# Performance work log

Hardware: AMD Instinct MI355X
Metric: run time of the kernel (lower is better)

## Reference

```python
import jax, jax.numpy as jnp
import numpy as np

D_MODEL = 1024
VOCAB = 32000
NUM_HEADS = 3  # MTP steps
NHEAD = 2      # attention heads per encoder layer
D_FF = 2048    # torch TransformerEncoderLayer default dim_feedforward
EPS_RMS = 1e-8
EPS_LN = 1e-5


def rmsnorm(x):
    rms = jnp.sqrt(jnp.mean(x * x, axis=-1, keepdims=True) + EPS_RMS)
    return x / rms


def layernorm(x, g, b):
    m = jnp.mean(x, axis=-1, keepdims=True)
    v = jnp.mean((x - m) ** 2, axis=-1, keepdims=True)
    return (x - m) / jnp.sqrt(v + EPS_LN) * g + b


def encoder_layer_single_token(x, p):
    # x: (..., d). Self-attention over a length-1 sequence: softmax over one key
    # gives attention weight 1, so attn_out = Wo @ (Wv @ x). Post-norm (torch default).
    v = x @ p['Wv'].T + p['bv']
    attn = v @ p['Wo'].T + p['bo']
    x = layernorm(x + attn, p['ln1_g'], p['ln1_b'])
    ff = jax.nn.relu(x @ p['W1'].T + p['b1']) @ p['W2'].T + p['b2']
    x = layernorm(x + ff, p['ln2_g'], p['ln2_b'])
    return x


def setup_inputs() -> dict:
    key = jax.random.key(0)
    ks = jax.random.split(key, 4)
    token_ids = jax.random.randint(ks[0], (4, 512), 0, VOCAB)
    embed = jax.random.normal(ks[1], (VOCAB, D_MODEL), dtype=jnp.float32) * 0.02
    s = 1.0 / np.sqrt(D_MODEL)
    params = []
    kk = ks[2]
    for k in range(NUM_HEADS):
        kk, *sub = jax.random.split(kk, 10)
        p = {
            'Wmerge': jax.random.normal(sub[0], (D_MODEL, 2 * D_MODEL)) * s,
            'bmerge': jnp.zeros((D_MODEL,)),
            'Wv': jax.random.normal(sub[1], (D_MODEL, D_MODEL)) * s,
            'bv': jnp.zeros((D_MODEL,)),
            'Wo': jax.random.normal(sub[2], (D_MODEL, D_MODEL)) * s,
            'bo': jnp.zeros((D_MODEL,)),
            'W1': jax.random.normal(sub[3], (D_FF, D_MODEL)) * s,
            'b1': jnp.zeros((D_FF,)),
            'W2': jax.random.normal(sub[4], (D_MODEL, D_FF)) * (1.0 / np.sqrt(D_FF)),
            'b2': jnp.zeros((D_MODEL,)),
            'ln1_g': jnp.ones((D_MODEL,)), 'ln1_b': jnp.zeros((D_MODEL,)),
            'ln2_g': jnp.ones((D_MODEL,)), 'ln2_b': jnp.zeros((D_MODEL,)),
        }
        params.append(p)
    # flatten params into dict entries layer{k}_{name}
    out = {'token_ids': token_ids, 'embed': embed}
    for k, p in enumerate(params):
        for name, val in p.items():
            out[f'l{k}_{name}'] = val
    return out


def _forward(token_ids, embed, layers):
    B, T = token_ids.shape
    embeds = embed[token_ids]              # (B, T, d)
    n_pos = T - NUM_HEADS                  # positions i = 0 .. T-NUM_HEADS-1
    # vectorize over i: h_prev starts as h0_seq[:, i, :] for all i at once
    idx = jnp.arange(n_pos)
    h_prev = embeds[:, idx, :]             # (B, P, d)
    logits_list = []
    for k in range(NUM_HEADS):
        p = layers[k]
        tok = embeds[:, idx + (k + 1), :]  # (B, P, d) future token embeds
        merged = jnp.concatenate([rmsnorm(h_prev), rmsnorm(tok)], axis=-1)  # (B,P,2d)
        x = merged @ p['Wmerge'].T + p['bmerge']                            # (B,P,d)
        h_curr = encoder_layer_single_token(x, p)
        logits = h_curr @ embed.T          # tied unembed (B,P,V)
        logits_list.append(logits)
        h_prev = h_curr
    # stack -> (B, P, NUM_HEADS, V) matching torch stack(dim=1) per-position then outer list
    return jnp.stack(logits_list, axis=2)


def reference(token_ids, embed,
              l0_Wmerge, l0_bmerge, l0_Wv, l0_bv, l0_Wo, l0_bo, l0_W1, l0_b1, l0_W2, l0_b2, l0_ln1_g, l0_ln1_b, l0_ln2_g, l0_ln2_b,
              l1_Wmerge, l1_bmerge, l1_Wv, l1_bv, l1_Wo, l1_bo, l1_W1, l1_b1, l1_W2, l1_b2, l1_ln1_g, l1_ln1_b, l1_ln2_g, l1_ln2_b,
              l2_Wmerge, l2_bmerge, l2_Wv, l2_bv, l2_Wo, l2_bo, l2_W1, l2_b1, l2_W2, l2_b2, l2_ln1_g, l2_ln1_b, l2_ln2_g, l2_ln2_b):
    names = ['Wmerge', 'bmerge', 'Wv', 'bv', 'Wo', 'bo', 'W1', 'b1', 'W2', 'b2', 'ln1_g', 'ln1_b', 'ln2_g', 'ln2_b']
    vals = [l0_Wmerge, l0_bmerge, l0_Wv, l0_bv, l0_Wo, l0_bo, l0_W1, l0_b1, l0_W2, l0_b2, l0_ln1_g, l0_ln1_b, l0_ln2_g, l0_ln2_b,
            l1_Wmerge, l1_bmerge, l1_Wv, l1_bv, l1_Wo, l1_bo, l1_W1, l1_b1, l1_W2, l1_b2, l1_ln1_g, l1_ln1_b, l1_ln2_g, l1_ln2_b,
            l2_Wmerge, l2_bmerge, l2_Wv, l2_bv, l2_Wo, l2_bo, l2_W1, l2_b1, l2_W2, l2_b2, l2_ln1_g, l2_ln1_b, l2_ln2_g, l2_ln2_b]
    layers = [dict(zip(names, vals[i * 14:(i + 1) * 14])) for i in range(NUM_HEADS)]
    return _forward(token_ids, embed, layers)
```

## Files before the change

### kernel.cpp

```cpp
#include <hip/hip_runtime.h>


#define NPOS   509
#define MROWS  2036
#define MPAD   2048
#define DMODEL 1024

typedef _Float16 f16;
typedef _Float16 f16x8 __attribute__((ext_vector_type(8)));
typedef _Float16 f16x4 __attribute__((ext_vector_type(4)));
typedef float    f32x4 __attribute__((ext_vector_type(4)));

#define MFMA16(a, b, c) __builtin_amdgcn_mfma_f32_16x16x32_f16(a, b, c, 0, 0, 0)
#define VM0  asm volatile("s_waitcnt vmcnt(0)" ::: "memory")
#define VM2  asm volatile("s_waitcnt vmcnt(2)" ::: "memory")
#define VM10 asm volatile("s_waitcnt vmcnt(10)" ::: "memory")
#define BAR  asm volatile("s_barrier" ::: "memory")

__device__ __forceinline__ void gld_lds16(const void* g, void* l) {
  __builtin_amdgcn_global_load_lds(
      (const __attribute__((address_space(1))) void*)g,
      (__attribute__((address_space(3))) void*)l, 16, 0, 0);
}

__global__ __launch_bounds__(256) void conv_f32_f16(const float* __restrict__ src,
                                                    f16* __restrict__ dst, long n) {
  long i = ((long)blockIdx.x * 256 + threadIdx.x) * 8;
  if (i + 8 <= n) {
    float4 a = *(const float4*)(src + i);
    float4 b = *(const float4*)(src + i + 4);
    f16x8 o = {(f16)a.x, (f16)a.y, (f16)a.z, (f16)a.w,
               (f16)b.x, (f16)b.y, (f16)b.z, (f16)b.w};
    *(f16x8*)(dst + i) = o;
  }
}

struct ConvArgs { const float* s[12]; f16* d[12]; long n[12]; };
__global__ __launch_bounds__(256) void conv_many(ConvArgs a) {
  int t = blockIdx.y;
  long i = ((long)blockIdx.x * 256 + threadIdx.x) * 8;
  if (i + 8 <= a.n[t]) {
    const float* src = a.s[t];
    float4 x = *(const float4*)(src + i);
    float4 y = *(const float4*)(src + i + 4);
    f16x8 o = {(f16)x.x, (f16)x.y, (f16)x.z, (f16)x.w,
               (f16)y.x, (f16)y.y, (f16)y.z, (f16)y.w};
    *(f16x8*)(a.d[t] + i) = o;
  }
}

struct TpArgs { const float* s[3]; f16* d[3]; };
__global__ __launch_bounds__(256) void transpose3(TpArgs a) {
  __shared__ float t[32][33];
  int h = blockIdx.z;
  int bx = blockIdx.x * 32, by = blockIdx.y * 32;
  int tx = threadIdx.x & 31, ty = threadIdx.x >> 5;
  const float* src = a.s[h];
  f16* dst = a.d[h];
  #pragma unroll
  for (int r = 0; r < 32; r += 8)
    t[ty + r][tx] = src[(long)(by + ty + r) * 1024 + bx + tx];
  __syncthreads();
  #pragma unroll
  for (int r = 0; r < 32; r += 8)
    dst[(long)(bx + ty + r) * 1024 + by + tx] = (f16)t[tx][ty + r];
}

struct BvoArgs { const float* Wo[3]; const float* bv[3]; const float* bo[3]; float* out[3]; };
__global__ __launch_bounds__(64) void make_bvo3(BvoArgs a) {
  int h = blockIdx.y, r = blockIdx.x, l = threadIdx.x;
  const float* Wo = a.Wo[h];
  const float* bv = a.bv[h];
  float s = 0.0f;
  for (int k = l; k < 1024; k += 64) s += Wo[(long)r * 1024 + k] * bv[k];
  #pragma unroll
  for (int off = 32; off > 0; off >>= 1) s += __shfl_xor(s, off);
  if (l == 0) a.out[h][r] = s + a.bo[h][r];
}

__device__ __forceinline__ float2 block_reduce2(float a, float b) {
  #pragma unroll
  for (int off = 32; off > 0; off >>= 1) {
    a += __shfl_xor(a, off);
    b += __shfl_xor(b, off);
  }
  __shared__ float2 red[4];
  int wv = threadIdx.x >> 6;
  if ((threadIdx.x & 63) == 0) red[wv] = make_float2(a, b);
  __syncthreads();
  float2 r0 = red[0], r1 = red[1], r2 = red[2], r3 = red[3];
  return make_float2(r0.x + r1.x + r2.x + r3.x, r0.y + r1.y + r2.y + r3.y);
}

__global__ __launch_bounds__(256) void merge_rms(const float* __restrict__ hprev,
                                                 const float* __restrict__ embed,
                                                 const int* __restrict__ tok,
                                                 f16* __restrict__ merged, int koff,
                                                 int hsel) {
  int r = blockIdx.x;
  int b = r / NPOS, t = r - b * NPOS;
  int tid = threadIdx.x;
  const float* hrow = (hsel >= 0)
      ? embed + (long)tok[b * 512 + t + hsel] * DMODEL
      : hprev + (long)r * DMODEL;
  float4 hv = ((const float4*)hrow)[tid];
  float4 tv = ((const float4*)(embed + (long)tok[b * 512 + t + koff] * DMODEL))[tid];
  float sh = hv.x * hv.x + hv.y * hv.y + hv.z * hv.z + hv.w * hv.w;
  float st = tv.x * tv.x + tv.y * tv.y + tv.z * tv.z + tv.w * tv.w;
  float2 tot = block_reduce2(sh, st);
  float ih = 1.0f / sqrtf(tot.x * (1.0f / DMODEL) + 1e-8f);
  float it = 1.0f / sqrtf(tot.y * (1.0f / DMODEL) + 1e-8f);
  f16x4 oh = {(f16)(hv.x * ih), (f16)(hv.y * ih), (f16)(hv.z * ih), (f16)(hv.w * ih)};
  f16x4 ot = {(f16)(tv.x * it), (f16)(tv.y * it), (f16)(tv.z * it), (f16)(tv.w * it)};
  *(f16x4*)(merged + (long)r * 2048 + tid * 4) = oh;
  *(f16x4*)(merged + (long)r * 2048 + 1024 + tid * 4) = ot;
}

__global__ __launch_bounds__(256) void add_ln(const float* __restrict__ x,
                                              const float* __restrict__ res,
                                              const float* __restrict__ g,
                                              const float* __restrict__ bb,
                                              float* __restrict__ yf,
                                              f16* __restrict__ yh) {
  int r = blockIdx.x, tid = threadIdx.x;
  float4 a = ((const float4*)(x + (long)r * DMODEL))[tid];
  float4 c = ((const float4*)(res + (long)r * DMODEL))[tid];
  a.x += c.x; a.y += c.y; a.z += c.z; a.w += c.w;
  float s  = a.x + a.y + a.z + a.w;
  float ss = a.x * a.x + a.y * a.y + a.z * a.z + a.w * a.w;
  float2 tot = block_reduce2(s, ss);
  float mean = tot.x * (1.0f / DMODEL);
  float var  = tot.y * (1.0f / DMODEL) - mean * mean;
  float inv  = 1.0f / sqrtf(var + 1e-5f);
  float4 gv = ((const float4*)g)[tid];
  float4 bv = ((const float4*)bb)[tid];
  float y0 = (a.x - mean) * inv * gv.x + bv.x;
  float y1 = (a.y - mean) * inv * gv.y + bv.y;
  float y2 = (a.z - mean) * inv * gv.z + bv.z;
  float y3 = (a.w - mean) * inv * gv.w + bv.w;
  float4 o = {y0, y1, y2, y3};
  ((float4*)(yf + (long)r * DMODEL))[tid] = o;
  f16x4 oh = {(f16)y0, (f16)y1, (f16)y2, (f16)y3};
  *(f16x4*)(yh + (long)r * DMODEL + tid * 4) = oh;
}

template <int HAS_BIAS, int RELU, int WF32, int WF16, int MASK>
__global__ __launch_bounds__(256) void gemm_sm(const f16* __restrict__ A,
                                               const f16* __restrict__ B,
                                               const float* __restrict__ bias,
                                               float* __restrict__ Cf,
                                               f16* __restrict__ Ch,
                                               int K, int N, long ldc, long coff,
                                               int mval, long zsA, long zsB, long zsC) {
  __shared__ __align__(16) f16 sA[3][2048];
  __shared__ __align__(16) f16 sB[3][2048];
  const int tid  = threadIdx.x;
  const int lane = tid & 63, wv = tid >> 6;
  const int wm = wv >> 1, wn = wv & 1;
  const int bm = blockIdx.y, bn = blockIdx.x;
  const int lr = lane & 15, lk = lane >> 4;

  A += (long)blockIdx.z * zsA;
  B += (long)blockIdx.z * zsB;
  Ch += (long)blockIdx.z * zsC;

  const f16* gA = A + ((long)(bm * 64 + (tid >> 2))) * K + (tid & 3) * 8;
  const f16* gB = B + ((long)(bn * 64 + (tid >> 2))) * K + (tid & 3) * 8;

  const int aoff = (wm * 32 + lr) * 32 + lk * 8;
  const int boff = (wn * 32 + lr) * 32 + lk * 8;

  f32x4 acc[2][2] = {};

#define SSTAGE(buf, kt)                                \
  gld_lds16(gA + (long)(kt) * 32, &sA[buf][tid * 8]);  \
  gld_lds16(gB + (long)(kt) * 32, &sB[buf][tid * 8]);

  const int nk = K >> 5;
  SSTAGE(0, 0);
  SSTAGE(1, 1);

  int cur = 0, stg = 2;
  for (int kt = 0; kt < nk; ++kt) {
    if (kt + 1 < nk) { VM2; } else { VM0; }
    BAR;
    if (kt + 2 < nk) { SSTAGE(stg, kt + 2); }
    f16x8 af0 = *(const f16x8*)&sA[cur][aoff];
    f16x8 af1 = *(const f16x8*)&sA[cur][aoff + 512];
    f16x8 bf0 = *(const f16x8*)&sB[cur][boff];
    f16x8 bf1 = *(const f16x8*)&sB[cur][boff + 512];
    acc[0][0] = MFMA16(af0, bf0, acc[0][0]);
    acc[0][1] = MFMA16(af0, bf1, acc[0][1]);
    acc[1][0] = MFMA16(af1, bf0, acc[1][0]);
    acc[1][1] = MFMA16(af1, bf1, acc[1][1]);
    cur = cur == 2 ? 0 : cur + 1;
    stg = stg == 2 ? 0 : stg + 1;
  }
#undef SSTAGE

  const int row0 = bm * 64 + wm * 32 + lk * 4;
  const int col0 = bn * 64 + wn * 32 + lr;
  #pragma unroll
  for (int mi = 0; mi < 2; ++mi) {
    #pragma unroll
    for (int ni = 0; ni < 2; ++ni) {
      int col = col0 + ni * 16;
      float bs = HAS_BIAS ? bias[col] : 0.0f;
      #pragma unroll
      for (int rg = 0; rg < 4; ++rg) {
        int row = row0 + mi * 16 + rg;
        if (!MASK || row < mval) {
          float v = acc[mi][ni][rg] + bs;
          if (RELU) v = v > 0.0f ? v : 0.0f;
          if (WF32) Cf[(long)row * ldc + coff + col] = v;
          if (WF16) Ch[(long)row * N + col] = (f16)v;
        }
      }
    }
  }
}

__global__ __launch_bounds__(512, 2) void gemm256x(const f16* __restrict__ A,
                                                   const f16* __restrict__ B,
                                                   float* __restrict__ C) {
  __shared__ __align__(16) f16 sA[4][8192];
  __shared__ __align__(16) f16 sB[4][8192];
  const int K = 1024;
  const int tid = threadIdx.x;
  const int lane = tid & 63;
  const int wv = tid >> 6;
  const int wm = wv >> 2, wn = wv & 3;
  const int lr = lane & 15, lk = lane >> 4;

  const int flat = blockIdx.y * 125 + blockIdx.x;
  const int xcd = flat & 7, idx = flat >> 3;
  const int bm = xcd * 3 + (idx % 3);
  const int bn = idx / 3;

  const int srow = tid >> 2;
  const int schunk = (tid & 3) ^ ((tid >> 3) & 3);
  const f16* gA = A + (long)(bm * 256 + srow) * K + schunk * 8;
  const f16* gB = B + (long)(bn * 256 + srow) * K + schunk * 8;
  const long rstep = 128L * (long)K;

  const int swz = ((lr >> 1) & 3) << 3;
  const int aoff = (((wm * 128 + lr) * 32) + lk * 8) ^ swz;
  const int boff = (((wn * 64  + lr) * 32) + lk * 8) ^ swz;

  f32x4 acc[8][4] = {};

#define STG_A(s, kt)                                            \
  gld_lds16(gA + (long)(kt) * 32, &sA[s][tid * 8]);             \
  gld_lds16(gA + (long)(kt) * 32 + rstep, &sA[s][tid * 8 + 4096]);
#define STG_B(s, kt)                                            \
  gld_lds16(gB + (long)(kt) * 32, &sB[s][tid * 8]);             \
  gld_lds16(gB + (long)(kt) * 32 + rstep, &sB[s][tid * 8 + 4096]);

  STG_A(0, 0); STG_B(0, 0);
  STG_A(1, 1); STG_B(1, 1);
  STG_A(2, 2); STG_B(2, 2);

  const int nt = 32;
  for (int t = 0; t < nt; ++t) {
    const int cur = t & 3, pre = (t + 3) & 3;
    const int kt = (t + 3 < nt) ? (t + 3) : 0;
    f16x8 af[8], bf[4];

    STG_A(pre, kt);
    VM10;
    BAR;
    #pragma unroll
    for (int mi = 0; mi < 8; ++mi) af[mi] = *(const f16x8*)&sA[cur][aoff + mi * 512];
    bf[0] = *(const f16x8*)&sB[cur][boff];
    bf[1] = *(const f16x8*)&sB[cur][boff + 512];
    __builtin_amdgcn_s_setprio(1);
    #pragma unroll
    for (int mi = 0; mi < 8; ++mi) {
      acc[mi][0] = MFMA16(af[mi], bf[0], acc[mi][0]);
      acc[mi][1] = MFMA16(af[mi], bf[1], acc[mi][1]);
    }
    __builtin_amdgcn_s_setprio(0);

    STG_B(pre, kt);
    bf[2] = *(const f16x8*)&sB[cur][boff + 1024];
    bf[3] = *(const f16x8*)&sB[cur][boff + 1536];
    __builtin_amdgcn_s_setprio(1);
    #pragma unroll
    for (int mi = 0; mi < 8; ++mi) {
      acc[mi][2] = MFMA16(af[mi], bf[2], acc[mi][2]);
      acc[mi][3] = MFMA16(af[mi], bf[3], acc[mi][3]);
    }
    __builtin_amdgcn_s_setprio(0);
    BAR;
  }
  VM0;

  const int head = bm >> 3;
  const long coff = (long)head * 32000;
  const int row0 = (bm & 7) * 256 + wm * 128 + lk * 4;
  const int col0 = bn * 256 + wn * 64 + lr;
  #pragma unroll
  for (int mi = 0; mi < 8; ++mi) {
    #pragma unroll
    for (int ni = 0; ni < 4; ++ni) {
      int col = col0 + ni * 16;
      #pragma unroll
      for (int rg = 0; rg < 4; ++rg) {
        int row = row0 + mi * 16 + rg;
        if (row < MROWS)
          __builtin_nontemporal_store(acc[mi][ni][rg],
                                      &C[(long)row * 96000 + coff + col]);
      }
    }
  }
#undef STG_A
#undef STG_B
}

extern "C" void kernel_launch(void* const* d_in, const int* in_sizes, int n_in,
                              void* d_out, int out_size, void* d_ws, size_t ws_size,
                              hipStream_t stream) {
  const int*   tok   = (const int*)d_in[0];
  const float* embed = (const float*)d_in[1];
  auto P = [&](int k, int j) { return (const float*)d_in[2 + k * 14 + j]; };
  float* out = (float*)d_out;

  char* w = (char*)d_ws;
  auto alloc = [&](size_t bytes) { char* p = w; w += bytes; return p; };
  const size_t MM = (size_t)1024 * 1024;

  f16* embed_h = (f16*)alloc((size_t)32000 * 1024 * 2);
  f16* Wo_all  = (f16*)alloc(3 * MM * 2);
  f16* Wvo_all = (f16*)alloc(3 * MM * 2);
  f16 *Wm_h[3], *W1_h[3], *W2_h[3];
  for (int k = 0; k < 3; ++k) {
    Wm_h[k]  = (f16*)alloc((size_t)1024 * 2048 * 2);
    W1_h[k]  = (f16*)alloc((size_t)2048 * 1024 * 2);
    W2_h[k]  = (f16*)alloc((size_t)1024 * 2048 * 2);
  }
  float* hprev  = (float*)alloc((size_t)MPAD * 1024 * 4);
  f16*   h_all  = (f16*)alloc((size_t)3 * MPAD * 1024 * 2);
  f16*   merged = (f16*)alloc((size_t)MPAD * 2048 * 2);
  float* xf     = (float*)alloc((size_t)MPAD * 1024 * 4);
  f16*   xh     = (f16*)alloc((size_t)MPAD * 1024 * 2);
  f16*   ff1    = (f16*)alloc((size_t)MPAD * 2048 * 2);
  float* t1     = (float*)alloc((size_t)MPAD * 1024 * 4);
  float* bvo    = (float*)alloc(3 * 1024 * 4);
  f16* WvT_all = merged;

  conv_f32_f16<<<16000, 256, 0, stream>>>(embed, embed_h, (long)32000 * 1024);

  ConvArgs ca;
  for (int k = 0; k < 3; ++k) {
    ca.s[k*4+0] = P(k, 0); ca.d[k*4+0] = Wm_h[k];        ca.n[k*4+0] = (long)1024 * 2048;
    ca.s[k*4+1] = P(k, 4); ca.d[k*4+1] = Wo_all + k*MM;  ca.n[k*4+1] = (long)1024 * 1024;
    ca.s[k*4+2] = P(k, 6); ca.d[k*4+2] = W1_h[k];        ca.n[k*4+2] = (long)2048 * 1024;
    ca.s[k*4+3] = P(k, 8); ca.d[k*4+3] = W2_h[k];        ca.n[k*4+3] = (long)1024 * 2048;
  }
  conv_many<<<dim3(1024, 12), 256, 0, stream>>>(ca);

  TpArgs ta;
  for (int k = 0; k < 3; ++k) { ta.s[k] = P(k, 2); ta.d[k] = WvT_all + k * MM; }
  transpose3<<<dim3(32, 32, 3), 256, 0, stream>>>(ta);

  gemm_sm<0, 0, 0, 1, 0><<<dim3(16, 16, 3), 256, 0, stream>>>(
      Wo_all, WvT_all, nullptr, nullptr, Wvo_all, 1024, 1024, 1024L, 0L, 1024,
      (long)MM, (long)MM, (long)MM);

  BvoArgs ba;
  for (int k = 0; k < 3; ++k) {
    ba.Wo[k] = P(k, 4); ba.bv[k] = P(k, 3); ba.bo[k] = P(k, 5); ba.out[k] = bvo + k * 1024;
  }
  make_bvo3<<<dim3(1024, 3), 64, 0, stream>>>(ba);

  for (int k = 0; k < 3; ++k) {
    merge_rms<<<MROWS, 256, 0, stream>>>(hprev, embed, tok, merged, k + 1,
                                         k == 0 ? 0 : -1);
    gemm_sm<1, 0, 1, 1, 0><<<dim3(16, 32), 256, 0, stream>>>(
        merged, Wm_h[k], P(k, 1), xf, xh, 2048, 1024, 1024L, 0L, MROWS, 0L, 0L, 0L);
    gemm_sm<1, 0, 1, 0, 0><<<dim3(16, 32), 256, 0, stream>>>(
        xh, Wvo_all + k * MM, bvo + k * 1024, t1, nullptr, 1024, 1024, 1024L, 0L,
        MROWS, 0L, 0L, 0L);
    add_ln<<<MROWS, 256, 0, stream>>>(xf, t1, P(k, 10), P(k, 11), xf, xh);
    gemm_sm<1, 1, 0, 1, 0><<<dim3(32, 32), 256, 0, stream>>>(
        xh, W1_h[k], P(k, 7), nullptr, ff1, 1024, 2048, 2048L, 0L, MROWS, 0L, 0L, 0L);
    gemm_sm<1, 0, 1, 0, 0><<<dim3(16, 32), 256, 0, stream>>>(
        ff1, W2_h[k], P(k, 9), t1, nullptr, 2048, 1024, 1024L, 0L, MROWS, 0L, 0L, 0L);
    add_ln<<<MROWS, 256, 0, stream>>>(xf, t1, P(k, 12), P(k, 13), hprev,
                                      h_all + (size_t)k * MPAD * 1024);
  }

  gemm256x<<<dim3(125, 24), 512, 0, stream>>>(h_all, embed_h, out);
}
```

Baseline: 1.004 ms.

## Restructure logits GEMM mainloop into double-buffered 64-wide K steps with ping-pong phases

Replaces the 4-stage, 32-wide-K LDS ring in the 256x256 logits GEMM with a 2-stage buffer holding 64-wide K tiles split into two halves. Each iteration runs four phases that interleave LDS fragment reads, async global-to-LDS prefetch of the next tile, and 16-MFMA blocks, separated by barriers, lgkmcnt waits and sched_barriers. The aim is a tighter overlap of memory and MFMA work with fewer loop iterations. The output store is also changed from nontemporal to a regular store. The cost is more barriers per iteration and a shallower prefetch depth.

```diff
diff --git a/kernel.cpp b/kernel.cpp
--- a/kernel.cpp
+++ b/kernel.cpp
@@ -12,10 +12,12 @@
 typedef float    f32x4 __attribute__((ext_vector_type(4)));
 
 #define MFMA16(a, b, c) __builtin_amdgcn_mfma_f32_16x16x32_f16(a, b, c, 0, 0, 0)
-#define VM0  asm volatile("s_waitcnt vmcnt(0)" ::: "memory")
-#define VM2  asm volatile("s_waitcnt vmcnt(2)" ::: "memory")
-#define VM10 asm volatile("s_waitcnt vmcnt(10)" ::: "memory")
-#define BAR  asm volatile("s_barrier" ::: "memory")
+#define VM0   asm volatile("s_waitcnt vmcnt(0)" ::: "memory")
+#define VM2   asm volatile("s_waitcnt vmcnt(2)" ::: "memory")
+#define VM4   asm volatile("s_waitcnt vmcnt(4)" ::: "memory")
+#define LGKM0 asm volatile("s_waitcnt lgkmcnt(0)" ::: "memory")
+#define SCHED0 __builtin_amdgcn_sched_barrier(0)
+#define BAR   asm volatile("s_barrier" ::: "memory")
 
 __device__ __forceinline__ void gld_lds16(const void* g, void* l) {
   __builtin_amdgcn_global_load_lds(
@@ -223,8 +225,8 @@
 __global__ __launch_bounds__(512, 2) void gemm256x(const f16* __restrict__ A,
                                                    const f16* __restrict__ B,
                                                    float* __restrict__ C) {
-  __shared__ __align__(16) f16 sA[4][8192];
-  __shared__ __align__(16) f16 sB[4][8192];
+  __shared__ __align__(16) f16 sA[2][2][8192];
+  __shared__ __align__(16) f16 sB[2][2][8192];
   const int K = 1024;
   const int tid = threadIdx.x;
   const int lane = tid & 63;
@@ -249,47 +251,78 @@
 
   f32x4 acc[8][4] = {};
 
-#define STG_A(s, kt)                                            \
-  gld_lds16(gA + (long)(kt) * 32, &sA[s][tid * 8]);             \
-  gld_lds16(gA + (long)(kt) * 32 + rstep, &sA[s][tid * 8 + 4096]);
-#define STG_B(s, kt)                                            \
-  gld_lds16(gB + (long)(kt) * 32, &sB[s][tid * 8]);             \
-  gld_lds16(gB + (long)(kt) * 32 + rstep, &sB[s][tid * 8 + 4096]);
-
-  STG_A(0, 0); STG_B(0, 0);
-  STG_A(1, 1); STG_B(1, 1);
-  STG_A(2, 2); STG_B(2, 2);
-
-  const int nt = 32;
+#define STG_A(s, h, ko)                                                  \
+  gld_lds16(gA + (ko) + (h) * 32, &sA[s][h][tid * 8]);                   \
+  gld_lds16(gA + (ko) + (h) * 32 + rstep, &sA[s][h][tid * 8 + 4096]);
+#define STG_B(s, h, ko)                                                  \
+  gld_lds16(gB + (ko) + (h) * 32, &sB[s][h][tid * 8]);                   \
+  gld_lds16(gB + (ko) + (h) * 32 + rstep, &sB[s][h][tid * 8 + 4096]);
+
+  STG_A(0, 0, 0); STG_B(0, 0, 0); STG_A(0, 1, 0); STG_B(0, 1, 0);
+  VM4;
+  BAR;
+
+  const int nt = 16;
   for (int t = 0; t < nt; ++t) {
-    const int cur = t & 3, pre = (t + 3) & 3;
-    const int kt = (t + 3 < nt) ? (t + 3) : 0;
-    f16x8 af[8], bf[4];
-
-    STG_A(pre, kt);
-    VM10;
+    const int cur = t & 1, nxt = cur ^ 1;
+    const long kn = (long)((t + 1 < nt) ? (t + 1) : 0) * 64;
+    f16x8 alo[4], ahi[4], bf[4];
+
+    #pragma unroll
+    for (int i = 0; i < 4; ++i) alo[i] = *(const f16x8*)&sA[cur][0][aoff + i * 512];
+    #pragma unroll
+    for (int j = 0; j < 4; ++j) bf[j] = *(const f16x8*)&sB[cur][0][boff + j * 512];
+    STG_A(nxt, 0, kn);
+    BAR; LGKM0; SCHED0;
+    __builtin_amdgcn_s_setprio(1);
+    #pragma unroll
+    for (int i = 0; i < 4; ++i)
+      #pragma unroll
+      for (int j = 0; j < 4; ++j)
+        acc[i][j] = MFMA16(alo[i], bf[j], acc[i][j]);
+    __builtin_amdgcn_s_setprio(0);
     BAR;
-    #pragma unroll
-    for (int mi = 0; mi < 8; ++mi) af[mi] = *(const f16x8*)&sA[cur][aoff + mi * 512];
-    bf[0] = *(const f16x8*)&sB[cur][boff];
-    bf[1] = *(const f16x8*)&sB[cur][boff + 512];
+
+    #pragma unroll
+    for (int i = 0; i < 4; ++i) ahi[i] = *(const f16x8*)&sA[cur][0][aoff + (i + 4) * 512];
+    STG_B(nxt, 0, kn);
+    VM4;
+    BAR; LGKM0; SCHED0;
     __builtin_amdgcn_s_setprio(1);
     #pragma unroll
-    for (int mi = 0; mi < 8; ++mi) {
-      acc[mi][0] = MFMA16(af[mi], bf[0], acc[mi][0]);
-      acc[mi][1] = MFMA16(af[mi], bf[1], acc[mi][1]);
-    }
+    for (int i = 0; i < 4; ++i)
+      #pragma unroll
+      for (int j = 0; j < 4; ++j)
+        acc[i + 4][j] = MFMA16(ahi[i], bf[j], acc[i + 4][j]);
     __builtin_amdgcn_s_setprio(0);
-
-    STG_B(pre, kt);
-    bf[2] = *(const f16x8*)&sB[cur][boff + 1024];
-    bf[3] = *(const f16x8*)&sB[cur][boff + 1536];
+    BAR;
+
+    #pragma unroll
+    for (int i = 0; i < 4; ++i) alo[i] = *(const f16x8*)&sA[cur][1][aoff + i * 512];
+    #pragma unroll
+    for (int j = 0; j < 4; ++j) bf[j] = *(const f16x8*)&sB[cur][1][boff + j * 512];
+    STG_A(nxt, 1, kn);
+    BAR; LGKM0; SCHED0;
     __builtin_amdgcn_s_setprio(1);
     #pragma unroll
-    for (int mi = 0; mi < 8; ++mi) {
-      acc[mi][2] = MFMA16(af[mi], bf[2], acc[mi][2]);
-      acc[mi][3] = MFMA16(af[mi], bf[3], acc[mi][3]);
-    }
+    for (int i = 0; i < 4; ++i)
+      #pragma unroll
+      for (int j = 0; j < 4; ++j)
+        acc[i][j] = MFMA16(alo[i], bf[j], acc[i][j]);
+    __builtin_amdgcn_s_setprio(0);
+    BAR;
+
+    #pragma unroll
+    for (int i = 0; i < 4; ++i) ahi[i] = *(const f16x8*)&sA[cur][1][aoff + (i + 4) * 512];
+    STG_B(nxt, 1, kn);
+    VM4;
+    BAR; LGKM0; SCHED0;
+    __builtin_amdgcn_s_setprio(1);
+    #pragma unroll
+    for (int i = 0; i < 4; ++i)
+      #pragma unroll
+      for (int j = 0; j < 4; ++j)
+        acc[i + 4][j] = MFMA16(ahi[i], bf[j], acc[i + 4][j]);
     __builtin_amdgcn_s_setprio(0);
     BAR;
   }
@@ -307,9 +340,7 @@
       #pragma unroll
       for (int rg = 0; rg < 4; ++rg) {
         int row = row0 + mi * 16 + rg;
-        if (row < MROWS)
-          __builtin_nontemporal_store(acc[mi][ni][rg],
-                                      &C[(long)row * 96000 + coff + col]);
+        if (row < MROWS) C[(long)row * 96000 + coff + col] = acc[mi][ni][rg];
       }
     }
   }
```

Result: no change. 992.6 us (-1.2%).
